# Kernel tuning notes

Measured on AMD Instinct MI355X. Metric: run time of the kernel, lower is better.

Reference implementation:

```python
import jax, jax.numpy as jnp
import numpy as np

N, E, F_IN, H, L = 100000, 1600000, 256, 128, 4
ALPHA, THETA, EPS = 0.1, 0.5, 1e-5


def setup_inputs() -> dict:
    key = jax.random.key(0)
    ks = jax.random.split(key, 6)
    x = jax.random.normal(ks[0], (N, F_IN), dtype=jnp.float32)
    edge_index = jax.random.randint(ks[1], (2, E), 0, N, dtype=jnp.int32)
    lin0_w = jax.random.normal(ks[2], (F_IN, H), dtype=jnp.float32) / np.sqrt(F_IN)
    lin0_b = jnp.zeros((H,), dtype=jnp.float32)
    conv_w = jax.random.normal(ks[3], (L, H, H), dtype=jnp.float32) / np.sqrt(H)
    bn_gamma = jnp.ones((L - 1, H), dtype=jnp.float32)
    bn_beta = jnp.zeros((L - 1, H), dtype=jnp.float32)
    return {"x": x, "edge_index": edge_index, "lin0_w": lin0_w, "lin0_b": lin0_b,
            "conv_w": conv_w, "bn_gamma": bn_gamma, "bn_beta": bn_beta}


def reference(x, edge_index, lin0_w, lin0_b, conv_w, bn_gamma, bn_beta):
    n = x.shape[0]
    loops = jnp.arange(n, dtype=edge_index.dtype)
    row = jnp.concatenate([edge_index[0], loops])  # source
    col = jnp.concatenate([edge_index[1], loops])  # target
    # GCN symmetric normalization with self-loops: D^{-1/2}(A+I)D^{-1/2}
    deg = jax.ops.segment_sum(jnp.ones_like(col, dtype=x.dtype), col, num_segments=n)
    dinv = jnp.where(deg > 0, jax.lax.rsqrt(deg), 0.0)
    norm = (dinv[row] * dinv[col])[:, None]  # [E+N, 1]

    def prop(h):  # sparse aggregation: out[c] += norm * h[r]
        return jax.ops.segment_sum(h[row] * norm, col, num_segments=n)

    # GCNConv input layer
    z = prop(x @ lin0_w) + lin0_b
    x0 = z
    for i in range(L):
        h = prop(z)
        beta = float(np.log(THETA / (i + 1) + 1.0))
        s = (1.0 - ALPHA) * h + ALPHA * x0          # identity mapping to initial features
        z = (1.0 - beta) * s + beta * (s @ conv_w[i])  # shared_weights GCN2Conv
        if i < L - 1:
            mu = jnp.mean(z, axis=0)
            var = jnp.mean((z - mu) ** 2, axis=0)
            z = (z - mu) * jax.lax.rsqrt(var + EPS) * bn_gamma[i] + bn_beta[i]
            z = jax.nn.relu(z)
    return z
```

## Files before the change

### kernel.cpp

```cpp
#include <hip/hip_runtime.h>
#include <hip/hip_bf16.h>
#include <math.h>

#define H 128
#define EPS_BN 1e-5f
#define RSTATS 16

typedef __attribute__((ext_vector_type(8))) short short8;
typedef __attribute__((ext_vector_type(4))) float f32x4;

__device__ __forceinline__ float bf2f(ushort u){
  union { float f; uint v; } x; x.v = ((uint)u) << 16; return x.f;
}
__device__ __forceinline__ ushort f2bf(float f){
  union { float f; uint v; } x; x.f = f;
  uint v = x.v;
  uint r = v + 0x7fff + ((v >> 16) & 1);
  return (ushort)(r >> 16);
}

__device__ __forceinline__ void acc8(float* a, uint4 v, float wt){
  a[0] += wt*bf2f((ushort)(v.x & 0xffff)); a[1] += wt*bf2f((ushort)(v.x >> 16));
  a[2] += wt*bf2f((ushort)(v.y & 0xffff)); a[3] += wt*bf2f((ushort)(v.y >> 16));
  a[4] += wt*bf2f((ushort)(v.z & 0xffff)); a[5] += wt*bf2f((ushort)(v.z >> 16));
  a[6] += wt*bf2f((ushort)(v.w & 0xffff)); a[7] += wt*bf2f((ushort)(v.w >> 16));
}


__global__ void k_count(const int* __restrict__ col, int E, int* __restrict__ cnt){
  int i = blockIdx.x*blockDim.x + threadIdx.x;
  if (i < E) atomicAdd(&cnt[col[i]], 1);
}

__global__ void k_scan1(const int* __restrict__ cnt, int* __restrict__ off,
                        int* __restrict__ bsum, float* __restrict__ dinv, int n){
  __shared__ int s[1024];
  int t = threadIdx.x;
  int i = blockIdx.x*1024 + t;
  int v = (i < n) ? cnt[i] : 0;
  if (i < n) dinv[i] = rsqrtf((float)v + 1.0f);
  s[t] = v; __syncthreads();
  for (int d = 1; d < 1024; d <<= 1){
    int x = (t >= d) ? s[t-d] : 0;
    __syncthreads();
    s[t] += x;
    __syncthreads();
  }
  if (i < n) off[i] = s[t] - v;
  if (t == 1023) bsum[blockIdx.x] = s[1023];
}

__global__ void k_scan2(int* bsum, int nb){
  int l = threadIdx.x;
  int carry = 0;
  for (int b0 = 0; b0 < nb; b0 += 64){
    int i = b0 + l;
    int orig = (i < nb) ? bsum[i] : 0;
    int v = orig;
    #pragma unroll
    for (int d = 1; d < 64; d <<= 1){
      int x = __shfl_up(v, d);
      if (l >= d) v += x;
    }
    if (i < nb) bsum[i] = carry + v - orig;
    carry += __shfl(v, 63);
  }
}

__global__ void k_scan3(int* __restrict__ off, int* __restrict__ cursor,
                        const int* __restrict__ bsum, int n, int Etot){
  int i = blockIdx.x*blockDim.x + threadIdx.x;
  if (i < n){ int o = off[i] + bsum[i >> 10]; off[i] = o; cursor[i] = o; }
  if (i == 0) off[n] = Etot;
}

__global__ void k_fill(const int* __restrict__ row, const int* __restrict__ col, int E,
                       const float* __restrict__ dinv, int* __restrict__ cursor,
                       uint2* __restrict__ edge){
  int i = blockIdx.x*blockDim.x + threadIdx.x;
  if (i < E){
    int c = col[i], r = row[i];
    int p = atomicAdd(&cursor[c], 1);
    edge[p] = make_uint2((uint)r, __float_as_uint(dinv[r]*dinv[c]));
  }
}


__global__ void k_prepw(const float* __restrict__ lin0_w, const float* __restrict__ conv_w,
                        ushort* __restrict__ lin0T, ushort* __restrict__ WpT,
                        float b0, float b1, float b2, float b3){
  int i = blockIdx.x*blockDim.x + threadIdx.x;
  if (i < 128*256){
    int nn = i >> 8, k = i & 255;
    lin0T[i] = f2bf(lin0_w[k*128 + nn]);
  } else if (i < 128*256 + 4*128*128){
    int j = i - 128*256;
    int ll = j >> 14, rc = j & 16383;
    int nn = rc >> 7, k = rc & 127;
    float beta = (ll==0)?b0:(ll==1)?b1:(ll==2)?b2:b3;
    float v = beta * conv_w[ll*16384 + k*128 + nn];
    if (k == nn) v += 1.0f - beta;
    WpT[j] = f2bf(v);
  }
}


__device__ __forceinline__ void gather_node(
    float* a, const ushort* __restrict__ zin, const uint2* __restrict__ edge,
    const float* __restrict__ dinv, int node, int e0, int e1, int lr){
  float wc = dinv[node]; wc *= wc;
  uint4 vs = *(const uint4*)(zin + (size_t)node*H + lr*8);
  int e = e0;
  int nfull = (e1 - e0) >> 2;
  if (nfull > 0){
    uint2 rc0 = edge[e], rc1 = edge[e+1], rc2 = edge[e+2], rc3 = edge[e+3];
    uint4 rv0 = *(const uint4*)(zin + (size_t)rc0.x*H + lr*8);
    uint4 rv1 = *(const uint4*)(zin + (size_t)rc1.x*H + lr*8);
    uint4 rv2 = *(const uint4*)(zin + (size_t)rc2.x*H + lr*8);
    uint4 rv3 = *(const uint4*)(zin + (size_t)rc3.x*H + lr*8);
    e += 4;
    for (int k = 1; k < nfull; ++k, e += 4){
      uint2 nc0 = edge[e], nc1 = edge[e+1], nc2 = edge[e+2], nc3 = edge[e+3];
      uint4 nv0 = *(const uint4*)(zin + (size_t)nc0.x*H + lr*8);
      uint4 nv1 = *(const uint4*)(zin + (size_t)nc1.x*H + lr*8);
      uint4 nv2 = *(const uint4*)(zin + (size_t)nc2.x*H + lr*8);
      uint4 nv3 = *(const uint4*)(zin + (size_t)nc3.x*H + lr*8);
      acc8(a, rv0, __uint_as_float(rc0.y));
      acc8(a, rv1, __uint_as_float(rc1.y));
      acc8(a, rv2, __uint_as_float(rc2.y));
      acc8(a, rv3, __uint_as_float(rc3.y));
      rc0 = nc0; rc1 = nc1; rc2 = nc2; rc3 = nc3;
      rv0 = nv0; rv1 = nv1; rv2 = nv2; rv3 = nv3;
    }
    acc8(a, rv0, __uint_as_float(rc0.y));
    acc8(a, rv1, __uint_as_float(rc1.y));
    acc8(a, rv2, __uint_as_float(rc2.y));
    acc8(a, rv3, __uint_as_float(rc3.y));
  }
  for (; e < e1; ++e){
    uint2 er = edge[e];
    uint4 v = *(const uint4*)(zin + (size_t)er.x*H + lr*8);
    acc8(a, v, __uint_as_float(er.y));
  }
  acc8(a, vs, wc);
}


__global__ __launch_bounds__(256) void k_prop0(
    const ushort* __restrict__ h, const int* __restrict__ off,
    const uint2* __restrict__ edge, const float* __restrict__ dinv,
    const float* __restrict__ bias,
    ushort* __restrict__ x0, int n){
  int gq = (blockIdx.x*blockDim.x + threadIdx.x) >> 4;
  if (gq >= n) return;
  int lr = threadIdx.x & 15;
  int e0 = off[gq], e1 = off[gq+1];
  float a[8];
  #pragma unroll
  for (int j = 0; j < 8; ++j) a[j] = 0.f;
  gather_node(a, h, edge, dinv, gq, e0, e1, lr);
  float4 b0 = *(const float4*)(bias + lr*8);
  float4 b1 = *(const float4*)(bias + lr*8 + 4);
  uint4 pk;
  pk.x = (uint)f2bf(a[0]+b0.x) | ((uint)f2bf(a[1]+b0.y) << 16);
  pk.y = (uint)f2bf(a[2]+b0.z) | ((uint)f2bf(a[3]+b0.w) << 16);
  pk.z = (uint)f2bf(a[4]+b1.x) | ((uint)f2bf(a[5]+b1.y) << 16);
  pk.w = (uint)f2bf(a[6]+b1.z) | ((uint)f2bf(a[7]+b1.w) << 16);
  *(uint4*)(x0 + (size_t)gq*H + lr*8) = pk;
}


template<bool STATS, bool OUTF32>
__global__ __launch_bounds__(256) void k_layer(
    const ushort* __restrict__ zin, const ushort* __restrict__ x0,
    const int* __restrict__ off, const uint2* __restrict__ edge,
    const float* __restrict__ dinv, const ushort* __restrict__ BT,
    void* __restrict__ zout, float* __restrict__ stats, int n)
{
  __shared__ ushort Sm[32*128];
  int t = threadIdx.x;
  int w = t >> 6, l = t & 63;
  int lr = l & 15, q = l >> 4;
  int base = blockIdx.x * 32;

  #pragma unroll
  for (int g2 = 0; g2 < 2; ++g2){
    int row  = w*8 + g2*4 + q;
    int node = base + row;
    float a[8];
    #pragma unroll
    for (int j = 0; j < 8; ++j) a[j] = 0.f;
    uint4 pk = make_uint4(0u,0u,0u,0u);
    if (node < n){
      int e0 = off[node], e1 = off[node+1];
      gather_node(a, zin, edge, dinv, node, e0, e1, lr);
      uint4 xv = *(const uint4*)(x0 + (size_t)node*H + lr*8);
      float s0 = 0.9f*a[0] + 0.1f*bf2f((ushort)(xv.x & 0xffff));
      float s1 = 0.9f*a[1] + 0.1f*bf2f((ushort)(xv.x >> 16));
      float s2 = 0.9f*a[2] + 0.1f*bf2f((ushort)(xv.y & 0xffff));
      float s3 = 0.9f*a[3] + 0.1f*bf2f((ushort)(xv.y >> 16));
      float s4 = 0.9f*a[4] + 0.1f*bf2f((ushort)(xv.z & 0xffff));
      float s5 = 0.9f*a[5] + 0.1f*bf2f((ushort)(xv.z >> 16));
      float s6 = 0.9f*a[6] + 0.1f*bf2f((ushort)(xv.w & 0xffff));
      float s7 = 0.9f*a[7] + 0.1f*bf2f((ushort)(xv.w >> 16));
      pk.x = (uint)f2bf(s0) | ((uint)f2bf(s1) << 16);
      pk.y = (uint)f2bf(s2) | ((uint)f2bf(s3) << 16);
      pk.z = (uint)f2bf(s4) | ((uint)f2bf(s5) << 16);
      pk.w = (uint)f2bf(s6) | ((uint)f2bf(s7) << 16);
    }
    *(uint4*)(&Sm[row*128 + ((lr ^ (row & 15))*8)]) = pk;
  }

  short8 bfr[2][4];
  #pragma unroll
  for (int c = 0; c < 2; ++c)
    #pragma unroll
    for (int ks = 0; ks < 4; ++ks)
      bfr[c][ks] = *(const short8*)(BT + (size_t)(w*32 + c*16 + lr)*H + ks*32 + q*8);

  __syncthreads();

  f32x4 acc[2][2];
  #pragma unroll
  for (int rt = 0; rt < 2; ++rt){
    acc[rt][0] = (f32x4){0.f,0.f,0.f,0.f};
    acc[rt][1] = (f32x4){0.f,0.f,0.f,0.f};
  }
  #pragma unroll
  for (int rt = 0; rt < 2; ++rt){
    int row = rt*16 + lr;
    #pragma unroll
    for (int ks = 0; ks < 4; ++ks){
      short8 af = *(const short8*)(&Sm[row*128 + (((ks*4 + q) ^ (row & 15))*8)]);
      acc[rt][0] = __builtin_amdgcn_mfma_f32_16x16x32_bf16(af, bfr[0][ks], acc[rt][0], 0,0,0);
      acc[rt][1] = __builtin_amdgcn_mfma_f32_16x16x32_bf16(af, bfr[1][ks], acc[rt][1], 0,0,0);
    }
  }

  #pragma unroll
  for (int rt = 0; rt < 2; ++rt){
    #pragma unroll
    for (int c = 0; c < 2; ++c){
      #pragma unroll
      for (int j = 0; j < 4; ++j){
        int row = base + rt*16 + q*4 + j;
        float v = acc[rt][c][j];
        if (OUTF32){
          if (row < n)
            ((float*)zout)[(size_t)row*H + w*32 + c*16 + lr] = v;
        } else {
          float other = __shfl(v, l ^ 1);
          if (!(lr & 1) && row < n){
            uint pk = (uint)f2bf(v) | ((uint)f2bf(other) << 16);
            ((uint*)zout)[(size_t)row*64 + w*16 + c*8 + (lr >> 1)] = pk;
          }
        }
      }
    }
  }
  if (STATS){
    #pragma unroll
    for (int c = 0; c < 2; ++c){
      float sv = 0.f, sq = 0.f;
      #pragma unroll
      for (int rt = 0; rt < 2; ++rt)
        #pragma unroll
        for (int j = 0; j < 4; ++j){
          float v = acc[rt][c][j];
          sv += v; sq += v*v;
        }
      sv += __shfl(sv, l ^ 16); sv += __shfl(sv, l ^ 32);
      sq += __shfl(sq, l ^ 16); sq += __shfl(sq, l ^ 32);
      if (q == 0){
        float* st = stats + (size_t)(blockIdx.x & (RSTATS-1))*256;
        atomicAdd(&st[w*32 + c*16 + lr], sv);
        atomicAdd(&st[128 + w*32 + c*16 + lr], sq);
      }
    }
  }
}


__global__ void k_bnfinal(float* __restrict__ stats, const float* __restrict__ gamma,
                          const float* __restrict__ beta, float* __restrict__ scsh,
                          float inv_n){
  int f = threadIdx.x;
  float s = 0.f, s2 = 0.f;
  for (int r = 0; r < RSTATS; ++r){
    s  += stats[r*256 + f];
    s2 += stats[r*256 + 128 + f];
    stats[r*256 + f] = 0.f;
    stats[r*256 + 128 + f] = 0.f;
  }
  float mu  = s * inv_n;
  float var = s2 * inv_n - mu*mu;
  float sc  = rsqrtf(var + EPS_BN) * gamma[f];
  scsh[f]       = sc;
  scsh[128 + f] = beta[f] - mu*sc;
}


__global__ __launch_bounds__(256) void k_bnapply(
    uint4* __restrict__ z, const float* __restrict__ scsh, int n16){
  int i = blockIdx.x*blockDim.x + threadIdx.x;
  if (i >= n16) return;
  int f8 = (i & 15) * 8;
  uint4 v = z[i];
  uint r[4];
  #pragma unroll
  for (int p = 0; p < 4; ++p){
    uint  u  = (&v.x)[p];
    float z0 = bf2f((ushort)(u & 0xffff));
    float z1 = bf2f((ushort)(u >> 16));
    float y0 = fmaxf(fmaf(z0, scsh[f8 + p*2],     scsh[128 + f8 + p*2]),     0.f);
    float y1 = fmaxf(fmaf(z1, scsh[f8 + p*2 + 1], scsh[128 + f8 + p*2 + 1]), 0.f);
    r[p] = (uint)f2bf(y0) | ((uint)f2bf(y1) << 16);
  }
  z[i] = make_uint4(r[0], r[1], r[2], r[3]);
}


__global__ __launch_bounds__(256) void k_gemm0(
    const float* __restrict__ Af, const ushort* __restrict__ BT,
    ushort* __restrict__ Cb, int n){
  const int K = 256;
  __shared__ ushort As[64*32];
  __shared__ ushort Bs[128*32];
  int t = threadIdx.x;
  int br = blockIdx.x * 64;
  int w = t >> 6, l = t & 63;
  int lr = l & 15, lk = l >> 4;
  int swz = (lr >> 1) & 3;

  f32x4 acc[8];
  #pragma unroll
  for (int i = 0; i < 8; ++i) acc[i] = (f32x4){0.f,0.f,0.f,0.f};

  int sar = t >> 2;
  int sab = t & 3;
  int sa_off = sar*32 + ((sab ^ ((sar>>1)&3))*8);

  for (int k0 = 0; k0 < K; k0 += 32){
    int grow = br + sar;
    float4 v0 = make_float4(0.f,0.f,0.f,0.f), v1 = v0;
    if (grow < n){
      v0 = *(const float4*)(Af + (size_t)grow*K + k0 + sab*8);
      v1 = *(const float4*)(Af + (size_t)grow*K + k0 + sab*8 + 4);
    }
    ushort tmp[8] = {f2bf(v0.x),f2bf(v0.y),f2bf(v0.z),f2bf(v0.w),
                     f2bf(v1.x),f2bf(v1.y),f2bf(v1.z),f2bf(v1.w)};
    *(uint4*)(&As[sa_off]) = *(const uint4*)tmp;
    #pragma unroll
    for (int i = 0; i < 2; ++i){
      int qq = t + i*256;
      int nrow = qq >> 2, bb = qq & 3;
      uint4 v = *(const uint4*)(BT + (size_t)nrow*K + k0 + bb*8);
      *(uint4*)(&Bs[nrow*32 + ((bb ^ ((nrow>>1)&3))*8)]) = v;
    }
    __syncthreads();
    short8 af = *(const short8*)(&As[(w*16+lr)*32 + ((lk ^ swz)*8)]);
    #pragma unroll
    for (int tn = 0; tn < 8; ++tn){
      short8 bfv = *(const short8*)(&Bs[(tn*16+lr)*32 + ((lk ^ swz)*8)]);
      acc[tn] = __builtin_amdgcn_mfma_f32_16x16x32_bf16(af, bfv, acc[tn], 0, 0, 0);
    }
    __syncthreads();
  }
  int orow = br + w*16 + lk*4;
  #pragma unroll
  for (int tn = 0; tn < 8; ++tn){
    #pragma unroll
    for (int j = 0; j < 4; ++j){
      float mine  = acc[tn][j];
      float other = __shfl(mine, l ^ 1);
      if (!(l & 1) && (orow + j) < n){
        uint pk = (uint)f2bf(mine) | ((uint)f2bf(other) << 16);
        ((uint*)Cb)[(size_t)(orow+j)*64 + tn*8 + (lr >> 1)] = pk;
      }
    }
  }
}


extern "C" void kernel_launch(void* const* d_in, const int* in_sizes, int n_in,
                              void* d_out, int out_size, void* d_ws, size_t ws_size,
                              hipStream_t stream){
  const float* x        = (const float*)d_in[0];
  const int*   ei       = (const int*)  d_in[1];
  const float* lin0_w   = (const float*)d_in[2];
  const float* lin0_b   = (const float*)d_in[3];
  const float* conv_w   = (const float*)d_in[4];
  const float* bn_gamma = (const float*)d_in[5];
  const float* bn_beta  = (const float*)d_in[6];
  float* out = (float*)d_out;

  int N = in_sizes[0] / 256;
  int E = in_sizes[1] / 2;
  const int* row = ei;
  const int* col = ei + E;

  char* ws = (char*)d_ws;
  size_t p = 0;
  auto alloc = [&](size_t bytes)->char*{
    char* r = ws + p; p = (p + bytes + 255) & ~(size_t)255; return r;
  };
  int*    cnt    = (int*)   alloc((size_t)N*4);
  int*    off    = (int*)   alloc((size_t)(N+1)*4);
  int*    cursor = (int*)   alloc((size_t)N*4);
  float*  dinv   = (float*) alloc((size_t)N*4);
  int*    bsum   = (int*)   alloc(512*4);
  uint2*  edge   = (uint2*) alloc((size_t)E*8);
  ushort* zb     = (ushort*)alloc((size_t)N*H*2);
  ushort* sb     = (ushort*)alloc((size_t)N*H*2);
  ushort* x0b    = (ushort*)alloc((size_t)N*H*2);
  ushort* lin0T  = (ushort*)alloc(128*256*2);
  ushort* WpT    = (ushort*)alloc(4*128*128*2);
  float*  stats  = (float*) alloc(RSTATS*256*4);
  float*  scsh   = (float*) alloc(2*128*4);

  float betas[4];
  for (int i = 0; i < 4; ++i) betas[i] = logf(0.5f/(float)(i+1) + 1.0f);
  float inv_n = 1.0f/(float)N;

  hipMemsetAsync(cnt, 0, (size_t)N*4, stream);
  k_count<<<(E+255)/256, 256, 0, stream>>>(col, E, cnt);
  int nb = (N + 1023)/1024;
  k_scan1<<<nb, 1024, 0, stream>>>(cnt, off, bsum, dinv, N);
  k_scan2<<<1, 64, 0, stream>>>(bsum, nb);
  k_scan3<<<(N+255)/256, 256, 0, stream>>>(off, cursor, bsum, N, E);
  k_fill <<<(E+255)/256, 256, 0, stream>>>(row, col, E, dinv, cursor, edge);

  k_prepw<<<(128*256 + 4*128*128 + 255)/256, 256, 0, stream>>>(
      lin0_w, conv_w, lin0T, WpT, betas[0], betas[1], betas[2], betas[3]);

  int gemm_blocks = (N + 63)/64;
  int lay_blocks  = (N + 31)/32;
  int prop_blocks = (N + 15)/16;
  int bn_blocks   = ((N*16) + 255)/256;

  k_gemm0<<<gemm_blocks, 256, 0, stream>>>(x, lin0T, sb, N);
  k_prop0<<<prop_blocks, 256, 0, stream>>>(sb, off, edge, dinv, lin0_b, x0b, N);

  hipMemsetAsync(stats, 0, RSTATS*256*4, stream);

  k_layer<true,false><<<lay_blocks, 256, 0, stream>>>(
      x0b, x0b, off, edge, dinv, WpT + 0*128*128, sb, stats, N);
  k_bnfinal<<<1, 128, 0, stream>>>(stats, bn_gamma + 0*H, bn_beta + 0*H, scsh, inv_n);
  k_bnapply<<<bn_blocks, 256, 0, stream>>>((uint4*)sb, scsh, N*16);

  k_layer<true,false><<<lay_blocks, 256, 0, stream>>>(
      sb, x0b, off, edge, dinv, WpT + 1*128*128, zb, stats, N);
  k_bnfinal<<<1, 128, 0, stream>>>(stats, bn_gamma + 1*H, bn_beta + 1*H, scsh, inv_n);
  k_bnapply<<<bn_blocks, 256, 0, stream>>>((uint4*)zb, scsh, N*16);

  k_layer<true,false><<<lay_blocks, 256, 0, stream>>>(
      zb, x0b, off, edge, dinv, WpT + 2*128*128, sb, stats, N);
  k_bnfinal<<<1, 128, 0, stream>>>(stats, bn_gamma + 2*H, bn_beta + 2*H, scsh, inv_n);
  k_bnapply<<<bn_blocks, 256, 0, stream>>>((uint4*)sb, scsh, N*16);

  k_layer<false,true><<<lay_blocks, 256, 0, stream>>>(
      sb, x0b, off, edge, dinv, WpT + 3*128*128, out, nullptr, N);
}
```

Measured before the change: 612.6 us.

## Gather neighbors with one wave per node using shuffled edge indices

Changes the sparse aggregation from 16 lanes per node (each loading 16 bytes per neighbor) to a full 64-lane wave per node. Each lane loads 4 bytes per neighbor. Edge records are fetched cooperatively, 16 per batch, and broadcast with shuffles; the next batch is prefetched. This is meant to raise memory-level parallelism and cut per-lane register pressure. In exchange, 4-byte loads replace wide loads, there is shuffle overhead, and the wave does wasted work on degrees that are not multiples of 16. Nodes in k_layer are now processed serially per wave rather than four at a time.

```diff
diff --git a/kernel.cpp b/kernel.cpp
--- a/kernel.cpp
+++ b/kernel.cpp
@@ -17,13 +17,6 @@
   uint v = x.v;
   uint r = v + 0x7fff + ((v >> 16) & 1);
   return (ushort)(r >> 16);
-}
-
-__device__ __forceinline__ void acc8(float* a, uint4 v, float wt){
-  a[0] += wt*bf2f((ushort)(v.x & 0xffff)); a[1] += wt*bf2f((ushort)(v.x >> 16));
-  a[2] += wt*bf2f((ushort)(v.y & 0xffff)); a[3] += wt*bf2f((ushort)(v.y >> 16));
-  a[4] += wt*bf2f((ushort)(v.z & 0xffff)); a[5] += wt*bf2f((ushort)(v.z >> 16));
-  a[6] += wt*bf2f((ushort)(v.w & 0xffff)); a[7] += wt*bf2f((ushort)(v.w >> 16));
 }
 
 
@@ -105,44 +98,44 @@
 }
 
 
-__device__ __forceinline__ void gather_node(
-    float* a, const ushort* __restrict__ zin, const uint2* __restrict__ edge,
-    const float* __restrict__ dinv, int node, int e0, int e1, int lr){
+__device__ __forceinline__ void gather_wave(
+    float& a0, float& a1, const ushort* __restrict__ zin,
+    const uint2* __restrict__ edge, const float* __restrict__ dinv,
+    int node, int e0, int e1, int l){
   float wc = dinv[node]; wc *= wc;
-  uint4 vs = *(const uint4*)(zin + (size_t)node*H + lr*8);
-  int e = e0;
-  int nfull = (e1 - e0) >> 2;
-  if (nfull > 0){
-    uint2 rc0 = edge[e], rc1 = edge[e+1], rc2 = edge[e+2], rc3 = edge[e+3];
-    uint4 rv0 = *(const uint4*)(zin + (size_t)rc0.x*H + lr*8);
-    uint4 rv1 = *(const uint4*)(zin + (size_t)rc1.x*H + lr*8);
-    uint4 rv2 = *(const uint4*)(zin + (size_t)rc2.x*H + lr*8);
-    uint4 rv3 = *(const uint4*)(zin + (size_t)rc3.x*H + lr*8);
-    e += 4;
-    for (int k = 1; k < nfull; ++k, e += 4){
-      uint2 nc0 = edge[e], nc1 = edge[e+1], nc2 = edge[e+2], nc3 = edge[e+3];
-      uint4 nv0 = *(const uint4*)(zin + (size_t)nc0.x*H + lr*8);
-      uint4 nv1 = *(const uint4*)(zin + (size_t)nc1.x*H + lr*8);
-      uint4 nv2 = *(const uint4*)(zin + (size_t)nc2.x*H + lr*8);
-      uint4 nv3 = *(const uint4*)(zin + (size_t)nc3.x*H + lr*8);
-      acc8(a, rv0, __uint_as_float(rc0.y));
-      acc8(a, rv1, __uint_as_float(rc1.y));
-      acc8(a, rv2, __uint_as_float(rc2.y));
-      acc8(a, rv3, __uint_as_float(rc3.y));
-      rc0 = nc0; rc1 = nc1; rc2 = nc2; rc3 = nc3;
-      rv0 = nv0; rv1 = nv1; rv2 = nv2; rv3 = nv3;
-    }
-    acc8(a, rv0, __uint_as_float(rc0.y));
-    acc8(a, rv1, __uint_as_float(rc1.y));
-    acc8(a, rv2, __uint_as_float(rc2.y));
-    acc8(a, rv3, __uint_as_float(rc3.y));
-  }
-  for (; e < e1; ++e){
-    uint2 er = edge[e];
-    uint4 v = *(const uint4*)(zin + (size_t)er.x*H + lr*8);
-    acc8(a, v, __uint_as_float(er.y));
-  }
-  acc8(a, vs, wc);
+  uint vs = *(const uint*)(zin + (size_t)node*H + l*2);
+  int deg = e1 - e0;
+  int lidx = l & 15;
+  uint2 rec = make_uint2(0u, 0u);
+  if (deg > 0){
+    int c = lidx < deg-1 ? lidx : deg-1;
+    rec = edge[e0 + c];
+  }
+  for (int c0 = 0; c0 < deg; c0 += 16){
+    uint2 cur = rec;
+    int nc0 = c0 + 16;
+    if (nc0 < deg){
+      int nrem = deg - nc0;
+      int c = lidx < nrem-1 ? lidx : nrem-1;
+      rec = edge[e0 + nc0 + c];
+    }
+    int cnt = deg - c0; if (cnt > 16) cnt = 16;
+    uint rows[16];
+    #pragma unroll
+    for (int k = 0; k < 16; ++k){
+      uint src = __shfl(cur.x, k);
+      rows[k] = *(const uint*)(zin + (size_t)src*H + l*2);
+    }
+    #pragma unroll
+    for (int k = 0; k < 16; ++k){
+      float wk = (k < cnt) ? __uint_as_float(__shfl(cur.y, k)) : 0.f;
+      uint v = rows[k];
+      a0 = fmaf(wk, bf2f((ushort)(v & 0xffff)), a0);
+      a1 = fmaf(wk, bf2f((ushort)(v >> 16)),   a1);
+    }
+  }
+  a0 = fmaf(wc, bf2f((ushort)(vs & 0xffff)), a0);
+  a1 = fmaf(wc, bf2f((ushort)(vs >> 16)),   a1);
 }
 
 
@@ -151,22 +144,14 @@
     const uint2* __restrict__ edge, const float* __restrict__ dinv,
     const float* __restrict__ bias,
     ushort* __restrict__ x0, int n){
-  int gq = (blockIdx.x*blockDim.x + threadIdx.x) >> 4;
-  if (gq >= n) return;
-  int lr = threadIdx.x & 15;
-  int e0 = off[gq], e1 = off[gq+1];
-  float a[8];
-  #pragma unroll
-  for (int j = 0; j < 8; ++j) a[j] = 0.f;
-  gather_node(a, h, edge, dinv, gq, e0, e1, lr);
-  float4 b0 = *(const float4*)(bias + lr*8);
-  float4 b1 = *(const float4*)(bias + lr*8 + 4);
-  uint4 pk;
-  pk.x = (uint)f2bf(a[0]+b0.x) | ((uint)f2bf(a[1]+b0.y) << 16);
-  pk.y = (uint)f2bf(a[2]+b0.z) | ((uint)f2bf(a[3]+b0.w) << 16);
-  pk.z = (uint)f2bf(a[4]+b1.x) | ((uint)f2bf(a[5]+b1.y) << 16);
-  pk.w = (uint)f2bf(a[6]+b1.z) | ((uint)f2bf(a[7]+b1.w) << 16);
-  *(uint4*)(x0 + (size_t)gq*H + lr*8) = pk;
+  int node = (blockIdx.x*blockDim.x + threadIdx.x) >> 6;
+  if (node >= n) return;
+  int l = threadIdx.x & 63;
+  float a0 = 0.f, a1 = 0.f;
+  gather_wave(a0, a1, h, edge, dinv, node, off[node], off[node+1], l);
+  float2 b = *(const float2*)(bias + l*2);
+  uint pk = (uint)f2bf(a0 + b.x) | ((uint)f2bf(a1 + b.y) << 16);
+  *(uint*)(x0 + (size_t)node*H + l*2) = pk;
 }
 
 
@@ -183,32 +168,21 @@
   int lr = l & 15, q = l >> 4;
   int base = blockIdx.x * 32;
 
-  #pragma unroll
-  for (int g2 = 0; g2 < 2; ++g2){
-    int row  = w*8 + g2*4 + q;
+  for (int nd = 0; nd < 8; ++nd){
+    int row  = w*8 + nd;
     int node = base + row;
-    float a[8];
-    #pragma unroll
-    for (int j = 0; j < 8; ++j) a[j] = 0.f;
-    uint4 pk = make_uint4(0u,0u,0u,0u);
+    uint pk = 0u;
     if (node < n){
-      int e0 = off[node], e1 = off[node+1];
-      gather_node(a, zin, edge, dinv, node, e0, e1, lr);
-      uint4 xv = *(const uint4*)(x0 + (size_t)node*H + lr*8);
-      float s0 = 0.9f*a[0] + 0.1f*bf2f((ushort)(xv.x & 0xffff));
-      float s1 = 0.9f*a[1] + 0.1f*bf2f((ushort)(xv.x >> 16));
-      float s2 = 0.9f*a[2] + 0.1f*bf2f((ushort)(xv.y & 0xffff));
-      float s3 = 0.9f*a[3] + 0.1f*bf2f((ushort)(xv.y >> 16));
-      float s4 = 0.9f*a[4] + 0.1f*bf2f((ushort)(xv.z & 0xffff));
-      float s5 = 0.9f*a[5] + 0.1f*bf2f((ushort)(xv.z >> 16));
-      float s6 = 0.9f*a[6] + 0.1f*bf2f((ushort)(xv.w & 0xffff));
-      float s7 = 0.9f*a[7] + 0.1f*bf2f((ushort)(xv.w >> 16));
-      pk.x = (uint)f2bf(s0) | ((uint)f2bf(s1) << 16);
-      pk.y = (uint)f2bf(s2) | ((uint)f2bf(s3) << 16);
-      pk.z = (uint)f2bf(s4) | ((uint)f2bf(s5) << 16);
-      pk.w = (uint)f2bf(s6) | ((uint)f2bf(s7) << 16);
-    }
-    *(uint4*)(&Sm[row*128 + ((lr ^ (row & 15))*8)]) = pk;
+      float a0 = 0.f, a1 = 0.f;
+      gather_wave(a0, a1, zin, edge, dinv, node, off[node], off[node+1], l);
+      uint xv = *(const uint*)(x0 + (size_t)node*H + l*2);
+      float s0 = 0.9f*a0 + 0.1f*bf2f((ushort)(xv & 0xffff));
+      float s1 = 0.9f*a1 + 0.1f*bf2f((ushort)(xv >> 16));
+      pk = (uint)f2bf(s0) | ((uint)f2bf(s1) << 16);
+    }
+    int j  = l >> 2;
+    int sw = j ^ (row & 15);
+    *(uint*)(&Sm[row*128 + sw*8 + (l & 3)*2]) = pk;
   }
 
   short8 bfr[2][4];
@@ -242,9 +216,9 @@
     #pragma unroll
     for (int c = 0; c < 2; ++c){
       #pragma unroll
-      for (int j = 0; j < 4; ++j){
-        int row = base + rt*16 + q*4 + j;
-        float v = acc[rt][c][j];
+      for (int j2 = 0; j2 < 4; ++j2){
+        int row = base + rt*16 + q*4 + j2;
+        float v = acc[rt][c][j2];
         if (OUTF32){
           if (row < n)
             ((float*)zout)[(size_t)row*H + w*32 + c*16 + lr] = v;
@@ -265,8 +239,8 @@
       #pragma unroll
       for (int rt = 0; rt < 2; ++rt)
         #pragma unroll
-        for (int j = 0; j < 4; ++j){
-          float v = acc[rt][c][j];
+        for (int j2 = 0; j2 < 4; ++j2){
+          float v = acc[rt][c][j2];
           sv += v; sq += v*v;
         }
       sv += __shfl(sv, l ^ 16); sv += __shfl(sv, l ^ 32);
@@ -435,7 +409,7 @@
 
   int gemm_blocks = (N + 63)/64;
   int lay_blocks  = (N + 31)/32;
-  int prop_blocks = (N + 15)/16;
+  int prop_blocks = (N + 3)/4;
   int bn_blocks   = ((N*16) + 255)/256;
 
   k_gemm0<<<gemm_blocks, 256, 0, stream>>>(x, lin0T, sb, N);
```

After: 683.3 us. +11.5%, slower.
